# Performance work log

Measured on AMD Instinct MI355X. Metric: run time of the kernel, lower is better.

## Reference

```python
import jax, jax.numpy as jnp
import numpy as np
from math import sqrt

HEADS = 16
D_MODEL = 1024
HEAD_DIM = D_MODEL // HEADS  # 64
B, SEQ = 2, 2048


def setup_inputs() -> dict:
    key = jax.random.key(0)
    ks = jax.random.split(key, 8)
    k = jax.random.normal(ks[0], (B, SEQ, D_MODEL), dtype=jnp.float32)
    q = jax.random.normal(ks[1], (B, SEQ, D_MODEL), dtype=jnp.float32)
    v = jax.random.normal(ks[2], (B, SEQ, D_MODEL), dtype=jnp.float32)
    # causal mask, broadcast over batch and heads; masked_fill where mask == 0
    mask = jnp.tril(jnp.ones((SEQ, SEQ), dtype=jnp.int32))[None, None, :, :]
    s = 1.0 / sqrt(HEAD_DIM)
    Wq = jax.random.normal(ks[3], (HEAD_DIM, HEAD_DIM), dtype=jnp.float32) * s
    Wk = jax.random.normal(ks[4], (HEAD_DIM, HEAD_DIM), dtype=jnp.float32) * s
    Wv = jax.random.normal(ks[5], (HEAD_DIM, HEAD_DIM), dtype=jnp.float32) * s
    Wo = jax.random.normal(ks[6], (D_MODEL, D_MODEL), dtype=jnp.float32) * (1.0 / sqrt(D_MODEL))
    bo = jax.random.normal(ks[7], (D_MODEL,), dtype=jnp.float32) * 0.01
    return {"key": k, "query": q, "value": v, "mask": mask,
            "Wq": Wq, "Wk": Wk, "Wv": Wv, "Wo": Wo, "bo": bo}


def reference(key, query, value, mask, Wq, Wk, Wv, Wo, bo):
    b, q_len, d = query.shape
    k_len = key.shape[1]
    hd = d // HEADS
    # reshape to [b, len, heads, head_dim]
    k = key.reshape(b, k_len, HEADS, hd)
    q = query.reshape(b, q_len, HEADS, hd)
    v = value.reshape(b, k_len, HEADS, hd)
    # per-head-dim Linear (weights shared across heads); torch Linear: y = x @ W.T
    k = jnp.einsum('bkhd,ed->bkhe', k, Wk)
    q = jnp.einsum('bqhd,ed->bqhe', q, Wq)
    v = jnp.einsum('bvhd,ed->bvhe', v, Wv)
    # full attention matrix [b, h, q, k]
    product = jnp.einsum('bqhd,bkhd->bhqk', q, k)
    # NOTE: original masks BEFORE scaling by 1/sqrt(head_dim)
    product = jnp.where(mask == 0, jnp.float32(-1e20), product)
    product = product / jnp.float32(sqrt(hd))
    score = jax.nn.softmax(product, axis=-1)
    out = jnp.einsum('bhqv,bvhd->bqhd', score, v).reshape(b, q_len, d)
    out = out @ Wo.T + bo
    return out
```

## Files before the change

kernel.cpp:

```cpp
#include <hip/hip_runtime.h>

typedef __bf16 bf16x8 __attribute__((ext_vector_type(8)));
typedef float  f32x4  __attribute__((ext_vector_type(4)));
typedef float  f32x16 __attribute__((ext_vector_type(16)));
typedef unsigned int uint32x4 __attribute__((ext_vector_type(4)));

#define MFMA16(a, b, c) __builtin_amdgcn_mfma_f32_16x16x32_bf16((a), (b), (c), 0, 0, 0)
#define MFMA32(a, b, c) __builtin_amdgcn_mfma_f32_32x32x16_bf16((a), (b), (c), 0, 0, 0)

#define CVTPK(d, x, y) asm("v_cvt_pk_bf16_f32 %0, %1, %2" : "=v"(d) : "v"(x), "v"(y))
#define PLSWAP(a, b)   asm("v_permlane32_swap_b32 %0, %1" : "+v"(a), "+v"(b))

#define BAR_KEEP_VMEM() asm volatile("s_waitcnt lgkmcnt(0)\n\ts_barrier" ::: "memory")

__device__ inline float fast_exp2(float x) {
#if __has_builtin(__builtin_amdgcn_exp2f)
    return __builtin_amdgcn_exp2f(x);
#else
    return exp2f(x);
#endif
}

constexpr int SEQ = 2048;
constexpr int DM  = 1024;
constexpr int NH  = 16;
constexpr int HD  = 64;
constexpr int BATCH = 2;

__device__ inline bf16x8 ld8_f32(const float* p) {
    f32x4 a = *(const f32x4*)p;
    f32x4 b = *(const f32x4*)(p + 4);
    bf16x8 r;
    r[0] = (__bf16)a[0]; r[1] = (__bf16)a[1]; r[2] = (__bf16)a[2]; r[3] = (__bf16)a[3];
    r[4] = (__bf16)b[0]; r[5] = (__bf16)b[1]; r[6] = (__bf16)b[2]; r[7] = (__bf16)b[3];
    return r;
}

__global__ __launch_bounds__(256)
void proj_kernel(const float* __restrict__ Xq, const float* __restrict__ Xk,
                 const float* __restrict__ Xv,
                 const float* __restrict__ Wq, const float* __restrict__ Wk,
                 const float* __restrict__ Wv,
                 __bf16* __restrict__ Qp, __bf16* __restrict__ Kp,
                 __bf16* __restrict__ Vp)
{
    const int tid  = threadIdx.x;
    const int w    = tid >> 6;
    const int lane = tid & 63;
    const int quad = lane >> 4;
    const int l16  = lane & 15;
    const int sblk = blockIdx.x;
    const int bh   = blockIdx.y;
    const int tz   = blockIdx.z;

    const float* X = (tz == 0) ? Xq : (tz == 1) ? Xk : Xv;
    const float* W = (tz == 0) ? Wq : (tz == 1) ? Wk : Wv;
    __bf16*      O = (tz == 0) ? Qp : (tz == 1) ? Kp : Vp;
    const float scale = (tz == 0) ? (0.125f * 1.44269504088896f) : 1.0f;

    const int b = bh >> 4, h = bh & 15;
    const int mrow = sblk * 64 + w * 16 + l16;

    const size_t xoff = (size_t)(b * SEQ + mrow) * DM + h * HD + quad * 8;
    bf16x8 a0 = ld8_f32(X + xoff);
    bf16x8 a1 = ld8_f32(X + xoff + 32);

    f32x4 acc[4];
    #pragma unroll
    for (int nt = 0; nt < 4; ++nt) {
        const size_t woff = (size_t)(nt * 16 + l16) * HD + quad * 8;
        bf16x8 b0 = ld8_f32(W + woff);
        bf16x8 b1 = ld8_f32(W + woff + 32);
        f32x4 c = {0.f, 0.f, 0.f, 0.f};
        c = MFMA16(a0, b0, c);
        c = MFMA16(a1, b1, c);
        acc[nt] = c;
    }

    __bf16* obase = O + (size_t)bh * SEQ * HD;
    #pragma unroll
    for (int nt = 0; nt < 4; ++nt) {
        #pragma unroll
        for (int r = 0; r < 4; ++r) {
            const int srow = sblk * 64 + w * 16 + quad * 4 + r;
            obase[(size_t)srow * HD + nt * 16 + l16] = (__bf16)(acc[nt][r] * scale);
        }
    }
}

__global__ __launch_bounds__(256, 2)
void attn_kernel(const __bf16* __restrict__ Qp, const __bf16* __restrict__ Kp,
                 const __bf16* __restrict__ Vp, __bf16* __restrict__ AO)
{
    __shared__ __align__(16) unsigned int K_lds[2][64 * 36];
    __shared__ __align__(16) unsigned int VT2[2][64 * 36];

    const int tid  = threadIdx.x;
    const int w    = tid >> 6;
    const int lane = tid & 63;
    const int hi   = lane >> 5;
    const int l32  = lane & 31;
    const int qg   = w >> 1;
    const int kg   = w & 1;

    const int L   = blockIdx.x;
    const int pr  = (L >> 3) & 15;
    const int bh  = (L & 7) + 8 * (L >> 7);

    const __bf16* Qb = Qp + (size_t)bh * SEQ * HD;
    const __bf16* Kb = Kp + (size_t)bh * SEQ * HD;
    const __bf16* Vb = Vp + (size_t)bh * SEQ * HD;

    const int krow = tid >> 3, kcol = tid & 7;
    const int jp = tid & 31, d0 = (tid >> 5) * 8;

    #pragma unroll
    for (int phase = 0; phase < 2; ++phase) {
        const int tile = (phase == 0) ? (31 - pr) : pr;
        const int q0   = tile * 64;
        const int nkc  = tile + 1;

        __syncthreads();

        const __bf16* qp = Qb + (size_t)(q0 + 32 * qg + l32) * HD + hi * 8;
        const bf16x8 qb0 = *(const bf16x8*)(qp);
        const bf16x8 qb1 = *(const bf16x8*)(qp + 16);
        const bf16x8 qb2 = *(const bf16x8*)(qp + 32);
        const bf16x8 qb3 = *(const bf16x8*)(qp + 48);

        f32x16 accO[2];
        #pragma unroll
        for (int et = 0; et < 2; ++et) {
            #pragma unroll
            for (int r = 0; r < 16; ++r) accO[et][r] = 0.f;
        }
        float rs0 = 0.f, rs1 = 0.f;

        uint32x4 kA0, kA1, vAl, vAh, kB0, kB1, vBl, vBh;
        kA0 = *(const uint32x4*)(Kb + (size_t)krow * HD + kcol * 8);
        kA1 = *(const uint32x4*)(Kb + (size_t)(krow + 32) * HD + kcol * 8);
        vAl = *(const uint32x4*)(Vb + (size_t)(2 * jp) * HD + d0);
        vAh = *(const uint32x4*)(Vb + (size_t)(2 * jp + 1) * HD + d0);
        if (nkc > 1) {
            kB0 = *(const uint32x4*)(Kb + (size_t)(64 + krow) * HD + kcol * 8);
            kB1 = *(const uint32x4*)(Kb + (size_t)(64 + krow + 32) * HD + kcol * 8);
            vBl = *(const uint32x4*)(Vb + (size_t)(64 + 2 * jp) * HD + d0);
            vBh = *(const uint32x4*)(Vb + (size_t)(64 + 2 * jp + 1) * HD + d0);
        }

        auto STEP = [&](int kc, int buf, uint32x4& kp0, uint32x4& kp1,
                        uint32x4& vl, uint32x4& vh) {
            *(uint32x4*)&K_lds[buf][krow * 36 + kcol * 4]        = kp0;
            *(uint32x4*)&K_lds[buf][(krow + 32) * 36 + kcol * 4] = kp1;
            #pragma unroll
            for (int i2 = 0; i2 < 4; ++i2) {
                const unsigned int va = vl[i2], vb = vh[i2];
                VT2[buf][(d0 + 2 * i2    ) * 36 + jp] = (va & 0xffffu) | (vb << 16);
                VT2[buf][(d0 + 2 * i2 + 1) * 36 + jp] = (va >> 16) | (vb & 0xffff0000u);
            }

            if (kc + 2 < nkc) {
                const size_t o = (size_t)(kc + 2) * 64;
                kp0 = *(const uint32x4*)(Kb + (o + krow) * HD + kcol * 8);
                kp1 = *(const uint32x4*)(Kb + (o + krow + 32) * HD + kcol * 8);
                vl  = *(const uint32x4*)(Vb + (o + 2 * jp) * HD + d0);
                vh  = *(const uint32x4*)(Vb + (o + 2 * jp + 1) * HD + d0);
            }
            BAR_KEEP_VMEM();

            if (!(kc == tile && qg == 0 && kg == 1)) {
                const __bf16* kp = (const __bf16*)&K_lds[buf][(32 * kg + l32) * 36] + hi * 8;
                f32x16 s;
                #pragma unroll
                for (int r = 0; r < 16; ++r) s[r] = 0.f;
                __builtin_amdgcn_s_setprio(1);
                s = MFMA32(*(const bf16x8*)(kp),      qb0, s);
                s = MFMA32(*(const bf16x8*)(kp + 16), qb1, s);
                s = MFMA32(*(const bf16x8*)(kp + 32), qb2, s);
                s = MFMA32(*(const bf16x8*)(kp + 48), qb3, s);
                __builtin_amdgcn_s_setprio(0);

                if (kc == tile && qg == kg) {
                    #pragma unroll
                    for (int r = 0; r < 16; ++r) {
                        const int cr = (r & 3) + 8 * (r >> 2) + 4 * hi;
                        if (cr > l32) s[r] = -1e30f;
                    }
                }

                float p[16];
                #pragma unroll
                for (int r = 0; r < 16; ++r) p[r] = fast_exp2(s[r]);
                #pragma unroll
                for (int r = 0; r < 8; ++r) { rs0 += p[2 * r]; rs1 += p[2 * r + 1]; }

                unsigned int w0, w1, w2, w3, w4, w5, w6, w7;
                CVTPK(w0, p[0],  p[1]);  CVTPK(w1, p[2],  p[3]);
                CVTPK(w2, p[4],  p[5]);  CVTPK(w3, p[6],  p[7]);
                CVTPK(w4, p[8],  p[9]);  CVTPK(w5, p[10], p[11]);
                CVTPK(w6, p[12], p[13]); CVTPK(w7, p[14], p[15]);
                PLSWAP(w0, w2); PLSWAP(w1, w3); PLSWAP(w4, w6); PLSWAP(w5, w7);
                uint32x4 u0 = {w0, w1, w2, w3};
                uint32x4 u1 = {w4, w5, w6, w7};
                const bf16x8 pa0 = *(const bf16x8*)&u0;
                const bf16x8 pa1 = *(const bf16x8*)&u1;

                __builtin_amdgcn_s_setprio(1);
                #pragma unroll
                for (int et = 0; et < 2; ++et) {
                    const __bf16* vp = (const __bf16*)&VT2[buf][(et * 32 + l32) * 36]
                                       + 32 * kg + hi * 8;
                    accO[et] = MFMA32(pa0, *(const bf16x8*)(vp),      accO[et]);
                    accO[et] = MFMA32(pa1, *(const bf16x8*)(vp + 16), accO[et]);
                }
                __builtin_amdgcn_s_setprio(0);
            }
        };

        for (int kc = 0; kc < nkc; kc += 2) {
            STEP(kc, 0, kA0, kA1, vAl, vAh);
            if (kc + 1 < nkc) STEP(kc + 1, 1, kB0, kB1, vBl, vBh);
        }

        __syncthreads();
        float* red = (float*)K_lds;
        float rsum = rs0 + rs1;
        if (kg == 1) {
            float* dst = red + (size_t)(qg * 64 + lane) * 33;
            #pragma unroll
            for (int r = 0; r < 16; ++r) { dst[r] = accO[0][r]; dst[16 + r] = accO[1][r]; }
            dst[32] = rsum;
        }
        __syncthreads();
        if (kg == 0) {
            const float* src = red + (size_t)(qg * 64 + lane) * 33;
            #pragma unroll
            for (int r = 0; r < 16; ++r) { accO[0][r] += src[r]; accO[1][r] += src[16 + r]; }
            rsum += src[32];
            const float rt  = rsum + __shfl_xor(rsum, 32, 64);
            const float ivq = 1.0f / rt;
            const int b = bh >> 4, h = bh & 15;
            #pragma unroll
            for (int r = 0; r < 16; ++r) {
                const int cr = (r & 3) + 8 * (r >> 2) + 4 * hi;
                const float iv = __shfl(ivq, cr, 64);
                __bf16* ao = AO + (size_t)(b * SEQ + q0 + 32 * qg + cr) * DM + h * HD;
                ao[l32]      = (__bf16)(accO[0][r] * iv);
                ao[32 + l32] = (__bf16)(accO[1][r] * iv);
            }
        }
    }
}

__global__ __launch_bounds__(256)
void wconv_kernel(const float* __restrict__ Wo, __bf16* __restrict__ Wb)
{
    const size_t i = ((size_t)blockIdx.x * 256 + threadIdx.x) * 8;
    *(bf16x8*)(Wb + i) = ld8_f32(Wo + i);
}

__global__ __launch_bounds__(256)
void ogemm_kernel(const __bf16* __restrict__ AO, const __bf16* __restrict__ Wb,
                  const float* __restrict__ bo, float* __restrict__ out)
{
    __shared__ __align__(16) unsigned int A_lds[2][64 * 36];
    __shared__ __align__(16) unsigned int B_lds[2][128 * 36];

    const int tid  = threadIdx.x;
    const int w    = tid >> 6;
    const int lane = tid & 63;
    const int quad = lane >> 4;
    const int l16  = lane & 15;
    const int m0   = blockIdx.x * 64;
    const int n0   = blockIdx.y * 128;

    const int row = tid >> 3, c = tid & 7;

    f32x4 acc[8];
    #pragma unroll
    for (int nt = 0; nt < 8; ++nt) { f32x4 z = {0.f,0.f,0.f,0.f}; acc[nt] = z; }

    uint32x4 aA[2], bA[4], aB[2], bB[4];
    #pragma unroll
    for (int i = 0; i < 2; ++i) {
        aA[i] = *(const uint32x4*)(AO + (size_t)(m0 + row + i * 32) * DM + c * 8);
        aB[i] = *(const uint32x4*)(AO + (size_t)(m0 + row + i * 32) * DM + 64 + c * 8);
    }
    #pragma unroll
    for (int i = 0; i < 4; ++i) {
        bA[i] = *(const uint32x4*)(Wb + (size_t)(n0 + row + i * 32) * DM + c * 8);
        bB[i] = *(const uint32x4*)(Wb + (size_t)(n0 + row + i * 32) * DM + 64 + c * 8);
    }

    auto GSTEP = [&](int kc, int buf, uint32x4 (&ap)[2], uint32x4 (&bp)[4]) {
        #pragma unroll
        for (int i = 0; i < 2; ++i)
            *(uint32x4*)&A_lds[buf][(row + i * 32) * 36 + c * 4] = ap[i];
        #pragma unroll
        for (int i = 0; i < 4; ++i)
            *(uint32x4*)&B_lds[buf][(row + i * 32) * 36 + c * 4] = bp[i];

        if (kc + 2 < DM / 64) {
            const size_t o = (size_t)(kc + 2) * 64;
            #pragma unroll
            for (int i = 0; i < 2; ++i)
                ap[i] = *(const uint32x4*)(AO + (size_t)(m0 + row + i * 32) * DM + o + c * 8);
            #pragma unroll
            for (int i = 0; i < 4; ++i)
                bp[i] = *(const uint32x4*)(Wb + (size_t)(n0 + row + i * 32) * DM + o + c * 8);
        }
        BAR_KEEP_VMEM();

        #pragma unroll
        for (int ks = 0; ks < 2; ++ks) {
            bf16x8 a = *(const bf16x8*)&A_lds[buf][(w * 16 + l16) * 36 + ks * 16 + quad * 4];
            #pragma unroll
            for (int nt = 0; nt < 8; ++nt) {
                bf16x8 bb = *(const bf16x8*)&B_lds[buf][(nt * 16 + l16) * 36 + ks * 16 + quad * 4];
                acc[nt] = MFMA16(a, bb, acc[nt]);
            }
        }
    };

    for (int kc = 0; kc < DM / 64; kc += 2) {
        GSTEP(kc,     0, aA, bA);
        GSTEP(kc + 1, 1, aB, bB);
    }

    #pragma unroll
    for (int nt = 0; nt < 8; ++nt) {
        const int n = n0 + nt * 16 + l16;
        const float bof = bo[n];
        #pragma unroll
        for (int r = 0; r < 4; ++r) {
            const int m = m0 + w * 16 + quad * 4 + r;
            out[(size_t)m * DM + n] = acc[nt][r] + bof;
        }
    }
}

extern "C" void kernel_launch(void* const* d_in, const int* in_sizes, int n_in,
                              void* d_out, int out_size, void* d_ws, size_t ws_size,
                              hipStream_t stream)
{
    const float* key   = (const float*)d_in[0];
    const float* query = (const float*)d_in[1];
    const float* value = (const float*)d_in[2];
    const float* Wq = (const float*)d_in[4];
    const float* Wk = (const float*)d_in[5];
    const float* Wv = (const float*)d_in[6];
    const float* Wo = (const float*)d_in[7];
    const float* bo = (const float*)d_in[8];

    const size_t per = (size_t)BATCH * NH * SEQ * HD;
    __bf16* Qp = (__bf16*)d_ws;
    __bf16* Kp = Qp + per;
    __bf16* Vp = Kp + per;
    __bf16* AO = Vp + per;
    __bf16* Wb = Kp;

    proj_kernel<<<dim3(SEQ / 64, BATCH * NH, 3), 256, 0, stream>>>(
        query, key, value, Wq, Wk, Wv, Qp, Kp, Vp);
    attn_kernel<<<dim3(16 * BATCH * NH), 256, 0, stream>>>(Qp, Kp, Vp, AO);
    wconv_kernel<<<dim3(DM * DM / (256 * 8)), 256, 0, stream>>>(Wo, Wb);
    ogemm_kernel<<<dim3(BATCH * SEQ / 64, DM / 128), 256, 0, stream>>>(
        AO, Wb, bo, (float*)d_out);
}
```

Baseline: 186.1 us.

## Retile output GEMM to 64x64 blocks with 32x32 MFMA and XCD-aware mapping

The output projection GEMM moves from 64x128 tiles built from 16x16x32 MFMAs to 64x64 tiles where each wave computes a 32x32 block with 32x32x16 MFMAs. The grid becomes one-dimensional and is swizzled so that blocks on the same XCD share rows of AO, which is meant to improve L2 reuse and double the block count for occupancy. The trade-off is more blocks re-reading the Wo tiles and lower arithmetic intensity per block.

```diff
diff --git a/kernel.cpp b/kernel.cpp
--- a/kernel.cpp
+++ b/kernel.cpp
@@ -264,62 +264,60 @@
                   const float* __restrict__ bo, float* __restrict__ out)
 {
     __shared__ __align__(16) unsigned int A_lds[2][64 * 36];
-    __shared__ __align__(16) unsigned int B_lds[2][128 * 36];
+    __shared__ __align__(16) unsigned int B_lds[2][64 * 36];
 
     const int tid  = threadIdx.x;
     const int w    = tid >> 6;
     const int lane = tid & 63;
-    const int quad = lane >> 4;
-    const int l16  = lane & 15;
-    const int m0   = blockIdx.x * 64;
-    const int n0   = blockIdx.y * 128;
+    const int hi   = lane >> 5;
+    const int l32  = lane & 31;
+    const int wm   = w >> 1;
+    const int wn   = w & 1;
+
+    const int L   = blockIdx.x;
+    const int xcd = L & 7;
+    const int r_  = L >> 3;
+    const int n0  = (r_ & 15) * 64;
+    const int m0  = (xcd * 8 + (r_ >> 4)) * 64;
 
     const int row = tid >> 3, c = tid & 7;
 
-    f32x4 acc[8];
-    #pragma unroll
-    for (int nt = 0; nt < 8; ++nt) { f32x4 z = {0.f,0.f,0.f,0.f}; acc[nt] = z; }
-
-    uint32x4 aA[2], bA[4], aB[2], bB[4];
+    f32x16 acc;
+    #pragma unroll
+    for (int r = 0; r < 16; ++r) acc[r] = 0.f;
+
+    uint32x4 aA[2], bA[2], aB[2], bB[2];
     #pragma unroll
     for (int i = 0; i < 2; ++i) {
         aA[i] = *(const uint32x4*)(AO + (size_t)(m0 + row + i * 32) * DM + c * 8);
+        bA[i] = *(const uint32x4*)(Wb + (size_t)(n0 + row + i * 32) * DM + c * 8);
         aB[i] = *(const uint32x4*)(AO + (size_t)(m0 + row + i * 32) * DM + 64 + c * 8);
-    }
-    #pragma unroll
-    for (int i = 0; i < 4; ++i) {
-        bA[i] = *(const uint32x4*)(Wb + (size_t)(n0 + row + i * 32) * DM + c * 8);
         bB[i] = *(const uint32x4*)(Wb + (size_t)(n0 + row + i * 32) * DM + 64 + c * 8);
     }
 
-    auto GSTEP = [&](int kc, int buf, uint32x4 (&ap)[2], uint32x4 (&bp)[4]) {
+    auto GSTEP = [&](int kc, int buf, uint32x4 (&ap)[2], uint32x4 (&bp)[2]) {
         #pragma unroll
-        for (int i = 0; i < 2; ++i)
+        for (int i = 0; i < 2; ++i) {
             *(uint32x4*)&A_lds[buf][(row + i * 32) * 36 + c * 4] = ap[i];
-        #pragma unroll
-        for (int i = 0; i < 4; ++i)
             *(uint32x4*)&B_lds[buf][(row + i * 32) * 36 + c * 4] = bp[i];
+        }
 
         if (kc + 2 < DM / 64) {
             const size_t o = (size_t)(kc + 2) * 64;
             #pragma unroll
-            for (int i = 0; i < 2; ++i)
+            for (int i = 0; i < 2; ++i) {
                 ap[i] = *(const uint32x4*)(AO + (size_t)(m0 + row + i * 32) * DM + o + c * 8);
-            #pragma unroll
-            for (int i = 0; i < 4; ++i)
                 bp[i] = *(const uint32x4*)(Wb + (size_t)(n0 + row + i * 32) * DM + o + c * 8);
+            }
         }
         BAR_KEEP_VMEM();
 
+        const __bf16* ap2 = (const __bf16*)&A_lds[buf][(wm * 32 + l32) * 36] + hi * 8;
+        const __bf16* bp2 = (const __bf16*)&B_lds[buf][(wn * 32 + l32) * 36] + hi * 8;
         #pragma unroll
-        for (int ks = 0; ks < 2; ++ks) {
-            bf16x8 a = *(const bf16x8*)&A_lds[buf][(w * 16 + l16) * 36 + ks * 16 + quad * 4];
-            #pragma unroll
-            for (int nt = 0; nt < 8; ++nt) {
-                bf16x8 bb = *(const bf16x8*)&B_lds[buf][(nt * 16 + l16) * 36 + ks * 16 + quad * 4];
-                acc[nt] = MFMA16(a, bb, acc[nt]);
-            }
-        }
+        for (int f = 0; f < 4; ++f)
+            acc = MFMA32(*(const bf16x8*)(ap2 + 16 * f),
+                         *(const bf16x8*)(bp2 + 16 * f), acc);
     };
 
     for (int kc = 0; kc < DM / 64; kc += 2) {
@@ -327,15 +325,12 @@
         GSTEP(kc + 1, 1, aB, bB);
     }
 
-    #pragma unroll
-    for (int nt = 0; nt < 8; ++nt) {
-        const int n = n0 + nt * 16 + l16;
-        const float bof = bo[n];
-        #pragma unroll
-        for (int r = 0; r < 4; ++r) {
-            const int m = m0 + w * 16 + quad * 4 + r;
-            out[(size_t)m * DM + n] = acc[nt][r] + bof;
-        }
+    const int n = n0 + wn * 32 + l32;
+    const float bof = bo[n];
+    #pragma unroll
+    for (int r = 0; r < 16; ++r) {
+        const int cr = (r & 3) + 8 * (r >> 2) + 4 * hi;
+        out[(size_t)(m0 + wm * 32 + cr) * DM + n] = acc[r] + bof;
     }
 }
 
@@ -363,6 +358,6 @@
         query, key, value, Wq, Wk, Wv, Qp, Kp, Vp);
     attn_kernel<<<dim3(16 * BATCH * NH), 256, 0, stream>>>(Qp, Kp, Vp, AO);
     wconv_kernel<<<dim3(DM * DM / (256 * 8)), 256, 0, stream>>>(Wo, Wb);
-    ogemm_kernel<<<dim3(BATCH * SEQ / 64, DM / 128), 256, 0, stream>>>(
+    ogemm_kernel<<<dim3(64 * 16), 256, 0, stream>>>(
         AO, Wb, bo, (float*)d_out);
 }
```

After: 183.8 us (median of 2 runs). About the same (-1.2%).
